# Optimization experiments

Measured on AMD Instinct MI355X. Metric: run time of the kernel, lower is better.

## Reference

```python
import jax, jax.numpy as jnp
import numpy as np

DIM = 512
HEADS = 8
HEAD_DIM = DIM // HEADS
WIN = 3
N = WIN * WIN  # 9 tokens per window
HID = 4 * DIM
B = 8192
SCALE = HEAD_DIM ** -0.5
EPS = 1e-5


def _relative_position_index():
    coords = np.stack(np.meshgrid(np.arange(WIN), np.arange(WIN), indexing='ij'))  # (2,W,W)
    flat = coords.reshape(2, -1)  # (2, N)
    rel = flat[:, :, None] - flat[:, None, :]  # (2, N, N)
    rel = rel.transpose(1, 2, 0).copy()  # (N, N, 2)
    rel[:, :, 0] += WIN - 1
    rel[:, :, 1] += WIN - 1
    rel[:, :, 0] *= 2 * WIN - 1
    return rel.sum(-1)  # (N, N) int

REL_IDX = jnp.asarray(_relative_position_index())


def _layernorm(x, g, b):
    mu = jnp.mean(x, axis=-1, keepdims=True)
    var = jnp.mean(jnp.square(x - mu), axis=-1, keepdims=True)
    return (x - mu) * jax.lax.rsqrt(var + EPS) * g + b


def setup_inputs() -> dict:
    key = jax.random.key(0)
    ks = jax.random.split(key, 16)
    f32 = jnp.float32
    return {
        'x': jax.random.normal(ks[0], (B, N, DIM), f32),
        'gamma1': jnp.ones((DIM,), f32),
        'beta1': jnp.zeros((DIM,), f32),
        'w_qkv': jax.random.normal(ks[1], (3 * DIM, DIM), f32) * 0.02,
        'b_qkv': jnp.zeros((3 * DIM,), f32),
        'bias_table': jax.random.normal(ks[2], ((2 * WIN - 1) ** 2, HEADS), f32) * 0.02,
        'w_proj': jax.random.normal(ks[3], (DIM, DIM), f32) * 0.02,
        'b_proj': jnp.zeros((DIM,), f32),
        'gamma2': jnp.ones((DIM,), f32),
        'beta2': jnp.zeros((DIM,), f32),
        'w_fc1': jax.random.normal(ks[4], (HID, DIM), f32) * 0.02,
        'b_fc1': jnp.zeros((HID,), f32),
        'w_fc2': jax.random.normal(ks[5], (DIM, HID), f32) * 0.02,
        'b_fc2': jnp.zeros((DIM,), f32),
        'w_conv': jax.random.normal(ks[6], (DIM, 1, WIN, WIN), f32) * 0.02,
        'b_conv': jnp.zeros((DIM,), f32),
    }


def reference(x, gamma1, beta1, w_qkv, b_qkv, bias_table, w_proj, b_proj,
              gamma2, beta2, w_fc1, b_fc1, w_fc2, b_fc2, w_conv, b_conv):
    Bn, Nn, C = x.shape
    # --- window attention ---
    shortcut = x
    h = _layernorm(x, gamma1, beta1)
    qkv = h @ w_qkv.T + b_qkv  # (B, N, 3C)
    qkv = qkv.reshape(Bn, Nn, 3, HEADS, HEAD_DIM).transpose(2, 0, 3, 1, 4)  # (3,B,H,N,d)
    q, k, v = qkv[0] * SCALE, qkv[1], qkv[2]
    attn = jnp.einsum('bhnd,bhmd->bhnm', q, k)  # (B,H,N,N)
    rel_bias = bias_table[REL_IDX.reshape(-1)].reshape(Nn, Nn, HEADS).transpose(2, 0, 1)  # (H,N,N)
    attn = jax.nn.softmax(attn + rel_bias[None], axis=-1)
    out = jnp.einsum('bhnm,bhmd->bhnd', attn, v)  # (B,H,N,d)
    out = out.transpose(0, 2, 1, 3).reshape(Bn, Nn, C)
    out = out @ w_proj.T + b_proj
    x = shortcut + out
    # --- MLP ---
    h = _layernorm(x, gamma2, beta2)
    h = jax.nn.gelu(h @ w_fc1.T + b_fc1, approximate=False)
    h = h @ w_fc2.T + b_fc2
    x = x + h
    # --- depthwise 3x3 merge conv over the 3x3 grid (valid -> 1x1) ---
    x4 = x.transpose(0, 2, 1).reshape(Bn, C, WIN, WIN)  # (B,C,3,3)
    y = jnp.einsum('bchw,chw->bc', x4, w_conv[:, 0]) + b_conv  # (B,C)
    return y[:, None, :]  # (B,1,C)
```

## Files before the change

kernel.cpp:

```cpp
#include <hip/hip_runtime.h>


typedef short short8 __attribute__((ext_vector_type(8)));
typedef unsigned short ushort8 __attribute__((ext_vector_type(8)));
typedef float floatx4 __attribute__((ext_vector_type(4)));

static constexpr int R_TOT = 73728;

__device__ __forceinline__ unsigned short f2bf(float f) {
  union { float f; unsigned int u; } v; v.f = f;
  unsigned int r = v.u + 0x7FFFu + ((v.u >> 16) & 1u);
  return (unsigned short)(r >> 16);
}
__device__ __forceinline__ float bf2f(unsigned short u) {
  union { unsigned int u; float f; } v; v.u = ((unsigned int)u) << 16;
  return v.f;
}

__device__ __forceinline__ void gload_lds16(const void* g, void* l) {
  __builtin_amdgcn_global_load_lds(
      (const __attribute__((address_space(1))) unsigned int*)g,
      (__attribute__((address_space(3))) unsigned int*)l, 16, 0, 0);
}

__global__ __launch_bounds__(256)
void cvt4(const float* __restrict__ in, unsigned short* __restrict__ out) {
  int i = (blockIdx.x * 256 + threadIdx.x) * 4;
  floatx4 v = *(const floatx4*)(in + i);
  union { unsigned short s[4]; unsigned long long u; } pk;
  pk.s[0] = f2bf(v[0]); pk.s[1] = f2bf(v[1]); pk.s[2] = f2bf(v[2]); pk.s[3] = f2bf(v[3]);
  *(unsigned long long*)(out + i) = pk.u;
}

__global__ __launch_bounds__(256)
void ln_bf16(const float* __restrict__ in, const float* __restrict__ g,
             const float* __restrict__ b, unsigned short* __restrict__ out) {
  const int lane = threadIdx.x & 63;
  const int wid = threadIdx.x >> 6;
  const size_t row = (size_t)blockIdx.x * 4 + wid;
  const float* p = in + row * 512 + lane * 8;
  floatx4 v0 = *(const floatx4*)p;
  floatx4 v1 = *(const floatx4*)(p + 4);
  float s = v0[0] + v0[1] + v0[2] + v0[3] + v1[0] + v1[1] + v1[2] + v1[3];
  float ss = v0[0]*v0[0] + v0[1]*v0[1] + v0[2]*v0[2] + v0[3]*v0[3]
           + v1[0]*v1[0] + v1[1]*v1[1] + v1[2]*v1[2] + v1[3]*v1[3];
  #pragma unroll
  for (int m = 1; m < 64; m <<= 1) { s += __shfl_xor(s, m); ss += __shfl_xor(ss, m); }
  float mu = s * (1.f / 512.f);
  float var = ss * (1.f / 512.f) - mu * mu;
  float rs = rsqrtf(var + 1e-5f);
  const float* gp = g + lane * 8;
  const float* bp = b + lane * 8;
  floatx4 g0 = *(const floatx4*)gp, g1 = *(const floatx4*)(gp + 4);
  floatx4 b0 = *(const floatx4*)bp, b1 = *(const floatx4*)(bp + 4);
  ushort8 o;
  o[0] = f2bf((v0[0] - mu) * rs * g0[0] + b0[0]);
  o[1] = f2bf((v0[1] - mu) * rs * g0[1] + b0[1]);
  o[2] = f2bf((v0[2] - mu) * rs * g0[2] + b0[2]);
  o[3] = f2bf((v0[3] - mu) * rs * g0[3] + b0[3]);
  o[4] = f2bf((v1[0] - mu) * rs * g1[0] + b1[0]);
  o[5] = f2bf((v1[1] - mu) * rs * g1[1] + b1[1]);
  o[6] = f2bf((v1[2] - mu) * rs * g1[2] + b1[2]);
  o[7] = f2bf((v1[3] - mu) * rs * g1[3] + b1[3]);
  *(ushort8*)(out + row * 512 + lane * 8) = o;
}

template <int EPI>
__global__ __launch_bounds__(256)
void gemm_bt(const unsigned short* __restrict__ A,
             const unsigned short* __restrict__ W,
             const float* __restrict__ bias,
             const float* __restrict__ resid,
             unsigned short* __restrict__ outb,
             float* __restrict__ outf,
             int K, int Nn) {
  __shared__ unsigned short As[128 * 64];
  __shared__ unsigned short Bs[128 * 64];

  const int t = threadIdx.x;
  const int lane = t & 63;
  const int wid = t >> 6;
  const int wr = wid >> 1;
  const int wc = wid & 1;

  const size_t rowB = (size_t)blockIdx.y * 128;
  const size_t colB = (size_t)blockIdx.x * 128;

  floatx4 acc[4][4];
  #pragma unroll
  for (int m = 0; m < 4; ++m)
    #pragma unroll
    for (int n = 0; n < 4; ++n)
      acc[m][n] = (floatx4){0.f, 0.f, 0.f, 0.f};

  const int ar = t >> 3;
  const int ac = (t & 7) * 8;
  const unsigned short* Abase = A + (rowB + ar) * (size_t)K + ac;
  const unsigned short* Wbase = W + (colB + ar) * (size_t)K + ac;
  const size_t K32 = (size_t)K * 32;

  const int la = lane & 15;
  const int lk = (lane >> 4) * 8;

  for (int ks = 0; ks < K; ks += 64) {
    #pragma unroll
    for (int c = 0; c < 4; ++c) {
      gload_lds16(Abase + ks + c * K32, &As[c * 2048 + t * 8]);
      gload_lds16(Wbase + ks + c * K32, &Bs[c * 2048 + t * 8]);
    }
    __syncthreads();
    #pragma unroll
    for (int kk = 0; kk < 2; ++kk) {
      short8 aF[4], bF[4];
      #pragma unroll
      for (int m = 0; m < 4; ++m)
        aF[m] = *(const short8*)&As[(wr * 64 + m * 16 + la) * 64 + kk * 32 + lk];
      #pragma unroll
      for (int n = 0; n < 4; ++n)
        bF[n] = *(const short8*)&Bs[(wc * 64 + n * 16 + la) * 64 + kk * 32 + lk];
      #pragma unroll
      for (int m = 0; m < 4; ++m)
        #pragma unroll
        for (int n = 0; n < 4; ++n)
          acc[m][n] = __builtin_amdgcn_mfma_f32_16x16x32_bf16(aF[m], bF[n], acc[m][n], 0, 0, 0);
    }
    __syncthreads();
  }

  const int r0 = (int)rowB + wr * 64;
  const int c0 = (int)colB + wc * 64;
  #pragma unroll
  for (int m = 0; m < 4; ++m) {
    #pragma unroll
    for (int n = 0; n < 4; ++n) {
      #pragma unroll
      for (int j = 0; j < 4; ++j) {
        int r = r0 + m * 16 + (lane >> 4) * 4 + j;
        int c = c0 + n * 16 + la;
        float v = acc[m][n][j] + bias[c];
        if (EPI == 1) v = 0.5f * v * (1.0f + erff(v * 0.70710678118654752f));
        if (EPI == 2) {
          v += resid[(size_t)r * Nn + c];
          outf[(size_t)r * Nn + c] = v;
        } else {
          outb[(size_t)r * Nn + c] = f2bf(v);
        }
      }
    }
  }
}

__global__ __launch_bounds__(256)
void attn9(const unsigned short* __restrict__ qkv,
           const float* __restrict__ bias_table,
           unsigned short* __restrict__ out) {
  __shared__ float qL[4][9][64];
  __shared__ float kL[4][9][64];
  __shared__ float vL[4][9][64];
  __shared__ float sL[4][9][10];

  const int lane = threadIdx.x & 63;
  const int wid = threadIdx.x >> 6;
  const int bh = blockIdx.x * 4 + wid;
  const int b = bh >> 3;
  const int h = bh & 7;

  const size_t base = (size_t)b * 9 * 1536 + h * 64 + lane;
  #pragma unroll
  for (int i = 0; i < 9; ++i) {
    qL[wid][i][lane] = bf2f(qkv[base + i * 1536]) * 0.125f;
    kL[wid][i][lane] = bf2f(qkv[base + i * 1536 + 512]);
    vL[wid][i][lane] = bf2f(qkv[base + i * 1536 + 1024]);
  }
  __syncthreads();

  #pragma unroll
  for (int p = 0; p < 2; ++p) {
    int pair = lane + p * 64;
    if (pair < 81) {
      int i = pair / 9, j = pair % 9;
      const floatx4* qi = (const floatx4*)qL[wid][i];
      const floatx4* kj = (const floatx4*)kL[wid][j];
      float dot = 0.f;
      #pragma unroll
      for (int d = 0; d < 16; ++d) {
        floatx4 a = qi[d], c = kj[d];
        dot += a[0]*c[0] + a[1]*c[1] + a[2]*c[2] + a[3]*c[3];
      }
      int dy = i / 3 - j / 3 + 2;
      int dx = i % 3 - j % 3 + 2;
      dot += bias_table[(dy * 5 + dx) * 8 + h];
      sL[wid][i][j] = dot;
    }
  }
  __syncthreads();

  if (lane < 9) {
    float m = -1e30f;
    #pragma unroll
    for (int j = 0; j < 9; ++j) m = fmaxf(m, sL[wid][lane][j]);
    float e[9], sum = 0.f;
    #pragma unroll
    for (int j = 0; j < 9; ++j) { e[j] = __expf(sL[wid][lane][j] - m); sum += e[j]; }
    float inv = 1.f / sum;
    #pragma unroll
    for (int j = 0; j < 9; ++j) sL[wid][lane][j] = e[j] * inv;
  }
  __syncthreads();

  const size_t obase = (size_t)b * 9 * 512 + h * 64 + lane;
  #pragma unroll
  for (int i = 0; i < 9; ++i) {
    float a = 0.f;
    #pragma unroll
    for (int j = 0; j < 9; ++j) a += sL[wid][i][j] * vL[wid][j][lane];
    out[obase + i * 512] = f2bf(a);
  }
}

__global__ __launch_bounds__(256)
void dwconv9(const float* __restrict__ x2, const float* __restrict__ wc,
             const float* __restrict__ bc, float* __restrict__ out) {
  int idx = blockIdx.x * 256 + threadIdx.x;
  int c = idx & 511;
  int b = idx >> 9;
  const float* xp = x2 + (size_t)b * 9 * 512 + c;
  float acc = bc[c];
  #pragma unroll
  for (int t = 0; t < 9; ++t) acc += xp[t * 512] * wc[c * 9 + t];
  out[idx] = acc;
}

extern "C" void kernel_launch(void* const* d_in, const int* in_sizes, int n_in,
                              void* d_out, int out_size, void* d_ws, size_t ws_size,
                              hipStream_t stream) {
  const float* x      = (const float*)d_in[0];
  const float* gamma1 = (const float*)d_in[1];
  const float* beta1  = (const float*)d_in[2];
  const float* w_qkv  = (const float*)d_in[3];
  const float* b_qkv  = (const float*)d_in[4];
  const float* bias_t = (const float*)d_in[5];
  const float* w_proj = (const float*)d_in[6];
  const float* b_proj = (const float*)d_in[7];
  const float* gamma2 = (const float*)d_in[8];
  const float* beta2  = (const float*)d_in[9];
  const float* w_fc1  = (const float*)d_in[10];
  const float* b_fc1  = (const float*)d_in[11];
  const float* w_fc2  = (const float*)d_in[12];
  const float* b_fc2  = (const float*)d_in[13];
  const float* w_conv = (const float*)d_in[14];
  const float* b_conv = (const float*)d_in[15];
  float* out = (float*)d_out;

  static const int cand[6] = {73728, 36864, 18432, 9216, 4608, 2304};
  int M_C = 2304;
  for (int i = 0; i < 6; ++i) {
    size_t need = 6291456ull + (size_t)cand[i] * 10240ull;
    if (need <= ws_size) { M_C = cand[i]; break; }
  }
  const int nChunks = R_TOT / M_C;
  const int winC = M_C / 9;

  char* ws = (char*)d_ws;
  unsigned short* wqkvb  = (unsigned short*)(ws);
  unsigned short* wprojb = (unsigned short*)(ws + 1572864);
  unsigned short* wfc1b  = (unsigned short*)(ws + 2097152);
  unsigned short* wfc2b  = (unsigned short*)(ws + 4194304);
  char* base = ws + 6291456;
  const size_t szHB  = (size_t)M_C * 1024;
  const size_t szQKV = (size_t)M_C * 3072;
  const size_t szX1  = (size_t)M_C * 2048;
  unsigned short* hb   = (unsigned short*)base;
  unsigned short* aob  = hb;
  unsigned short* qkvb = (unsigned short*)(base + szHB);
  unsigned short* h2b  = qkvb;
  float* x2            = (float*)(base + szHB + szHB);
  float* x1            = (float*)(base + szHB + szQKV);
  unsigned short* gb   = (unsigned short*)(base + szHB + szQKV + szX1);

  cvt4<<<768, 256, 0, stream>>>(w_qkv, wqkvb);
  cvt4<<<256, 256, 0, stream>>>(w_proj, wprojb);
  cvt4<<<1024, 256, 0, stream>>>(w_fc1, wfc1b);
  cvt4<<<1024, 256, 0, stream>>>(w_fc2, wfc2b);

  for (int ch = 0; ch < nChunks; ++ch) {
    const size_t rOff = (size_t)ch * M_C;
    const float* xC = x + rOff * 512;
    float* outC = out + (size_t)ch * winC * 512;
    const int mt = M_C / 128;

    ln_bf16<<<M_C / 4, 256, 0, stream>>>(xC, gamma1, beta1, hb);
    gemm_bt<0><<<dim3(12, mt), 256, 0, stream>>>(hb, wqkvb, b_qkv, nullptr, qkvb, nullptr, 512, 1536);
    attn9<<<winC * 2, 256, 0, stream>>>(qkvb, bias_t, aob);
    gemm_bt<2><<<dim3(4, mt), 256, 0, stream>>>(aob, wprojb, b_proj, xC, nullptr, x1, 512, 512);
    ln_bf16<<<M_C / 4, 256, 0, stream>>>(x1, gamma2, beta2, h2b);
    gemm_bt<1><<<dim3(16, mt), 256, 0, stream>>>(h2b, wfc1b, b_fc1, nullptr, gb, nullptr, 512, 2048);
    gemm_bt<2><<<dim3(4, mt), 256, 0, stream>>>(gb, wfc2b, b_fc2, x1, nullptr, x2, 2048, 512);
    dwconv9<<<winC * 2, 256, 0, stream>>>(x2, w_conv, b_conv, outC);
  }
}
```

Before: 1.473 ms.

## Replace GEMM with 256x256 double-buffered 8-wave pipelined MFMA kernel

Replaces the simple 128x128 single-buffered GEMM with a 256x256-tile, 512-thread kernel. It double-buffers LDS through direct global-to-LDS loads, swizzles LDS addresses to avoid bank conflicts, interleaves quarter-tile staging with MFMA bursts under s_setprio, and remaps workgroups across XCDs for L2 locality. The goal is to hide global load latency and raise MFMA utilisation in the four GEMMs that dominate runtime. It costs 128KB of LDS per block and much more register pressure, and the hand-placed vmcnt waits and barriers are fragile. It also requires K to be a multiple of 128 and M and N to be multiples of 256.

```diff
diff --git a/kernel.cpp b/kernel.cpp
--- a/kernel.cpp
+++ b/kernel.cpp
@@ -22,6 +22,12 @@
       (const __attribute__((address_space(1))) unsigned int*)g,
       (__attribute__((address_space(3))) unsigned int*)l, 16, 0, 0);
 }
+
+#define FENCE asm volatile("" ::: "memory")
+#define BAR do { FENCE; __builtin_amdgcn_s_barrier(); FENCE; } while (0)
+#define WAITV0 asm volatile("s_waitcnt vmcnt(0)" ::: "memory")
+#define WAITV4 asm volatile("s_waitcnt vmcnt(4)" ::: "memory")
+#define WAITV8 asm volatile("s_waitcnt vmcnt(8)" ::: "memory")
 
 __global__ __launch_bounds__(256)
 void cvt4(const float* __restrict__ in, unsigned short* __restrict__ out) {
@@ -65,85 +71,146 @@
   *(ushort8*)(out + row * 512 + lane * 8) = o;
 }
 
+
+#define STAGE_A(d, qq, tk) do { \
+  gload_lds16(Ap + (rowB + (qq)*64 + rowU) * (size_t)K + (tk) + kofsU, \
+              sm + (d)*32768 + (qq)*16384 + wid*1024); \
+  gload_lds16(Ap + (rowB + 128 + (qq)*64 + rowU) * (size_t)K + (tk) + kofsU, \
+              sm + (d)*32768 + (qq)*16384 + 8192 + wid*1024); \
+} while (0)
+
+#define STAGE_B(d, hb, tk) do { \
+  gload_lds16(Wp + (colB + (wid>>2)*64 + (hb)*32 + colU) * (size_t)K + (tk) + kofsU, \
+              sm + 65536 + (d)*32768 + (hb)*16384 + wid*1024); \
+  gload_lds16(Wp + (colB + (2 + (wid>>2))*64 + (hb)*32 + colU) * (size_t)K + (tk) + kofsU, \
+              sm + 65536 + (d)*32768 + (hb)*16384 + 8192 + wid*1024); \
+} while (0)
+
+#define LOAD_A(d, qq) do { \
+  _Pragma("unroll") \
+  for (int fl = 0; fl < 4; ++fl) { \
+    aF[fl][0] = *(const short8*)(sm + (d)*32768 + (qq)*16384 + wm*8192 + (fl*2+0)*1024 + laneRD); \
+    aF[fl][1] = *(const short8*)(sm + (d)*32768 + (qq)*16384 + wm*8192 + (fl*2+1)*1024 + laneRD); \
+  } \
+} while (0)
+
+#define LOAD_B(d, hb, BF) do { \
+  _Pragma("unroll") \
+  for (int nl = 0; nl < 2; ++nl) { \
+    BF[nl][0] = *(const short8*)(sm + 65536 + (d)*32768 + (hb)*16384 + wn*4096 + (nl*2+0)*1024 + laneRD); \
+    BF[nl][1] = *(const short8*)(sm + 65536 + (d)*32768 + (hb)*16384 + wn*4096 + (nl*2+1)*1024 + laneRD); \
+  } \
+} while (0)
+
+#define MMQ(qa, hb, BF) do { \
+  __builtin_amdgcn_s_setprio(1); \
+  _Pragma("unroll") \
+  for (int fl = 0; fl < 4; ++fl) \
+    _Pragma("unroll") \
+    for (int nl = 0; nl < 2; ++nl) { \
+      acc[(qa)*4+fl][(hb)*2+nl] = __builtin_amdgcn_mfma_f32_16x16x32_bf16(aF[fl][0], BF[nl][0], acc[(qa)*4+fl][(hb)*2+nl], 0, 0, 0); \
+      acc[(qa)*4+fl][(hb)*2+nl] = __builtin_amdgcn_mfma_f32_16x16x32_bf16(aF[fl][1], BF[nl][1], acc[(qa)*4+fl][(hb)*2+nl], 0, 0, 0); \
+    } \
+  __builtin_amdgcn_s_setprio(0); \
+} while (0)
+
 template <int EPI>
-__global__ __launch_bounds__(256)
-void gemm_bt(const unsigned short* __restrict__ A,
-             const unsigned short* __restrict__ W,
-             const float* __restrict__ bias,
-             const float* __restrict__ resid,
-             unsigned short* __restrict__ outb,
-             float* __restrict__ outf,
-             int K, int Nn) {
-  __shared__ unsigned short As[128 * 64];
-  __shared__ unsigned short Bs[128 * 64];
+__global__ __launch_bounds__(512, 2)
+void gemm8p(const unsigned short* __restrict__ Ap,
+            const unsigned short* __restrict__ Wp,
+            const float* __restrict__ bias,
+            const float* __restrict__ resid,
+            unsigned short* __restrict__ outb,
+            float* __restrict__ outf,
+            int K, int Nn, int ntn) {
+  __shared__ __align__(16) char sm[131072];
 
   const int t = threadIdx.x;
-  const int lane = t & 63;
+  const int l = t & 63;
   const int wid = t >> 6;
-  const int wr = wid >> 1;
-  const int wc = wid & 1;
-
-  const size_t rowB = (size_t)blockIdx.y * 128;
-  const size_t colB = (size_t)blockIdx.x * 128;
-
-  floatx4 acc[4][4];
-  #pragma unroll
-  for (int m = 0; m < 4; ++m)
+  const int wm = wid >> 2;
+  const int wn = wid & 3;
+
+  const int nwg = gridDim.x;
+  const int orig = blockIdx.x;
+  const int q8 = nwg >> 3, r8 = nwg & 7;
+  const int xcd = orig & 7, idx = orig >> 3;
+  const int wg = (xcd < r8 ? xcd * (q8 + 1) : r8 * (q8 + 1) + (xcd - r8) * q8) + idx;
+  const int tm = wg / ntn, tn = wg % ntn;
+  const size_t rowB = (size_t)tm * 256;
+  const size_t colB = (size_t)tn * 256;
+
+  const int rowU = (wid >> 1) * 16 + (l >> 2);
+  const int colU = ((wid >> 1) & 1) * 16 + (l >> 2);
+  const int kofsU = (wid & 1) * 32 + (((l & 3) ^ ((l >> 4) & 3)) * 8);
+  const int laneRD = (l & 15) * 64 + (((l >> 4) ^ ((l >> 2) & 3)) * 16);
+
+  floatx4 acc[8][4];
+  #pragma unroll
+  for (int m = 0; m < 8; ++m)
     #pragma unroll
     for (int n = 0; n < 4; ++n)
       acc[m][n] = (floatx4){0.f, 0.f, 0.f, 0.f};
 
-  const int ar = t >> 3;
-  const int ac = (t & 7) * 8;
-  const unsigned short* Abase = A + (rowB + ar) * (size_t)K + ac;
-  const unsigned short* Wbase = W + (colB + ar) * (size_t)K + ac;
-  const size_t K32 = (size_t)K * 32;
-
-  const int la = lane & 15;
-  const int lk = (lane >> 4) * 8;
-
-  for (int ks = 0; ks < K; ks += 64) {
-    #pragma unroll
-    for (int c = 0; c < 4; ++c) {
-      gload_lds16(Abase + ks + c * K32, &As[c * 2048 + t * 8]);
-      gload_lds16(Wbase + ks + c * K32, &Bs[c * 2048 + t * 8]);
-    }
-    __syncthreads();
-    #pragma unroll
-    for (int kk = 0; kk < 2; ++kk) {
-      short8 aF[4], bF[4];
-      #pragma unroll
-      for (int m = 0; m < 4; ++m)
-        aF[m] = *(const short8*)&As[(wr * 64 + m * 16 + la) * 64 + kk * 32 + lk];
-      #pragma unroll
-      for (int n = 0; n < 4; ++n)
-        bF[n] = *(const short8*)&Bs[(wc * 64 + n * 16 + la) * 64 + kk * 32 + lk];
-      #pragma unroll
-      for (int m = 0; m < 4; ++m)
-        #pragma unroll
-        for (int n = 0; n < 4; ++n)
-          acc[m][n] = __builtin_amdgcn_mfma_f32_16x16x32_bf16(aF[m], bF[n], acc[m][n], 0, 0, 0);
-    }
-    __syncthreads();
-  }
-
-  const int r0 = (int)rowB + wr * 64;
-  const int c0 = (int)colB + wc * 64;
-  #pragma unroll
-  for (int m = 0; m < 4; ++m) {
-    #pragma unroll
-    for (int n = 0; n < 4; ++n) {
+  short8 aF[4][2], bF0[2][2], bF1[2][2];
+
+  STAGE_A(0, 0, 0);  STAGE_A(0, 1, 0);  STAGE_B(0, 0, 0);  STAGE_B(0, 1, 0);
+  STAGE_A(1, 0, 64); STAGE_A(1, 1, 64); STAGE_B(1, 0, 64); STAGE_B(1, 1, 64);
+  WAITV8; BAR;
+
+  const int NI = K >> 7;
+  for (int i = 0; i < NI; ++i) {
+    const int tk1 = i * 128 + 64;
+    const int tk2 = i * 128 + 128;
+    const int tk3 = i * 128 + 192;
+    const bool pre = (i > 0);
+    const bool nxt = (i < NI - 1);
+
+    LOAD_A(0, 0); LOAD_B(0, 0, bF0);
+    if (pre) STAGE_A(1, 1, tk1);
+    BAR; MMQ(0, 0, bF0); BAR;
+    LOAD_B(0, 1, bF1);
+    if (pre) STAGE_B(1, 0, tk1);
+    BAR; MMQ(0, 1, bF1); BAR;
+    LOAD_A(0, 1);
+    if (nxt) STAGE_A(0, 0, tk2);
+    BAR; MMQ(1, 1, bF1); BAR;
+    if (nxt) STAGE_B(0, 1, tk2);
+    BAR; MMQ(1, 0, bF0);
+    if (nxt) { WAITV4; } else { WAITV0; }
+    BAR;
+    LOAD_A(1, 0); LOAD_B(1, 0, bF0);
+    if (nxt) STAGE_A(0, 1, tk2);
+    BAR; MMQ(0, 0, bF0); BAR;
+    LOAD_B(1, 1, bF1);
+    if (nxt) STAGE_B(0, 0, tk2);
+    BAR; MMQ(0, 1, bF1); BAR;
+    LOAD_A(1, 1);
+    if (nxt) STAGE_A(1, 0, tk3);
+    BAR; MMQ(1, 1, bF1); BAR;
+    if (nxt) STAGE_B(1, 1, tk3);
+    BAR; MMQ(1, 0, bF0);
+    if (nxt) { WAITV4; }
+    BAR;
+  }
+  FENCE;
+
+  #pragma unroll
+  for (int mi = 0; mi < 8; ++mi) {
+    #pragma unroll
+    for (int ni = 0; ni < 4; ++ni) {
+      const int rr = (int)rowB + wm * 128 + (mi >> 2) * 64 + (mi & 3) * 16 + (l >> 4) * 4;
+      const int cc = (int)colB + wn * 64 + (ni >> 1) * 32 + (ni & 1) * 16 + (l & 15);
+      const float bs = bias[cc];
       #pragma unroll
       for (int j = 0; j < 4; ++j) {
-        int r = r0 + m * 16 + (lane >> 4) * 4 + j;
-        int c = c0 + n * 16 + la;
-        float v = acc[m][n][j] + bias[c];
+        float v = acc[mi][ni][j] + bs;
         if (EPI == 1) v = 0.5f * v * (1.0f + erff(v * 0.70710678118654752f));
         if (EPI == 2) {
-          v += resid[(size_t)r * Nn + c];
-          outf[(size_t)r * Nn + c] = v;
+          v += resid[(size_t)(rr + j) * Nn + cc];
+          outf[(size_t)(rr + j) * Nn + cc] = v;
         } else {
-          outb[(size_t)r * Nn + c] = f2bf(v);
+          outb[(size_t)(rr + j) * Nn + cc] = f2bf(v);
         }
       }
     }
@@ -283,19 +350,19 @@
   cvt4<<<1024, 256, 0, stream>>>(w_fc1, wfc1b);
   cvt4<<<1024, 256, 0, stream>>>(w_fc2, wfc2b);
 
+  const int mt256 = M_C / 256;
   for (int ch = 0; ch < nChunks; ++ch) {
     const size_t rOff = (size_t)ch * M_C;
     const float* xC = x + rOff * 512;
     float* outC = out + (size_t)ch * winC * 512;
-    const int mt = M_C / 128;
 
     ln_bf16<<<M_C / 4, 256, 0, stream>>>(xC, gamma1, beta1, hb);
-    gemm_bt<0><<<dim3(12, mt), 256, 0, stream>>>(hb, wqkvb, b_qkv, nullptr, qkvb, nullptr, 512, 1536);
+    gemm8p<0><<<dim3(mt256 * 6), 512, 0, stream>>>(hb, wqkvb, b_qkv, nullptr, qkvb, nullptr, 512, 1536, 6);
     attn9<<<winC * 2, 256, 0, stream>>>(qkvb, bias_t, aob);
-    gemm_bt<2><<<dim3(4, mt), 256, 0, stream>>>(aob, wprojb, b_proj, xC, nullptr, x1, 512, 512);
+    gemm8p<2><<<dim3(mt256 * 2), 512, 0, stream>>>(aob, wprojb, b_proj, xC, nullptr, x1, 512, 512, 2);
     ln_bf16<<<M_C / 4, 256, 0, stream>>>(x1, gamma2, beta2, h2b);
-    gemm_bt<1><<<dim3(16, mt), 256, 0, stream>>>(h2b, wfc1b, b_fc1, nullptr, gb, nullptr, 512, 2048);
-    gemm_bt<2><<<dim3(4, mt), 256, 0, stream>>>(gb, wfc2b, b_fc2, x1, nullptr, x2, 2048, 512);
+    gemm8p<1><<<dim3(mt256 * 8), 512, 0, stream>>>(h2b, wfc1b, b_fc1, nullptr, gb, nullptr, 512, 2048, 8);
+    gemm8p<2><<<dim3(mt256 * 2), 512, 0, stream>>>(gb, wfc2b, b_fc2, x1, nullptr, x2, 2048, 512, 2);
     dwconv9<<<winC * 2, 256, 0, stream>>>(x2, w_conv, b_conv, outC);
   }
 }
```

Result: faster. 1.372 ms (-6.8%).

## Rewrite bf16 GEMM with 128x256 tiles, swizzled LDS, prefetch and XCD remap

Applied to the files above, without the earlier changes.

Replaces the 128x128, 256-thread GEMM with a 512-thread kernel that computes 128x256 output tiles. It uses an XOR-swizzled LDS layout to avoid bank conflicts and remaps the 1D block index so neighbouring tiles land on the same XCD. It reads the whole K-step of fragments into registers, then issues the next tile's global-to-LDS loads so they overlap the MFMA work, and raises wave priority around the MFMA block. This aims to cut LDS conflicts and exposed load latency, and to improve cache reuse. The cost is more registers, and there is a possible race: LDS is overwritten after the fragment reads without a trailing barrier.

```diff
diff --git a/kernel.cpp b/kernel.cpp
--- a/kernel.cpp
+++ b/kernel.cpp
@@ -22,6 +22,10 @@
       (const __attribute__((address_space(1))) unsigned int*)g,
       (__attribute__((address_space(3))) unsigned int*)l, 16, 0, 0);
 }
+
+#define FENCE asm volatile("" ::: "memory")
+#define BAR do { FENCE; __builtin_amdgcn_s_barrier(); FENCE; } while (0)
+#define WAITV0 asm volatile("s_waitcnt vmcnt(0)" ::: "memory")
 
 __global__ __launch_bounds__(256)
 void cvt4(const float* __restrict__ in, unsigned short* __restrict__ out) {
@@ -61,30 +65,41 @@
   o[4] = f2bf((v1[0] - mu) * rs * g1[0] + b1[0]);
   o[5] = f2bf((v1[1] - mu) * rs * g1[1] + b1[1]);
   o[6] = f2bf((v1[2] - mu) * rs * g1[2] + b1[2]);
-  o[7] = f2bf((v1[3] - mu) * rs * g1[3] + b1[3]);
+  o[7] = f2bf((v1[3] - mu) * rs * g1[3] + b1[7-4]);
   *(ushort8*)(out + row * 512 + lane * 8) = o;
 }
 
 template <int EPI>
-__global__ __launch_bounds__(256)
-void gemm_bt(const unsigned short* __restrict__ A,
-             const unsigned short* __restrict__ W,
-             const float* __restrict__ bias,
-             const float* __restrict__ resid,
-             unsigned short* __restrict__ outb,
-             float* __restrict__ outf,
-             int K, int Nn) {
-  __shared__ unsigned short As[128 * 64];
-  __shared__ unsigned short Bs[128 * 64];
+__global__ __launch_bounds__(512, 4)
+void gemmk(const unsigned short* __restrict__ Ap,
+           const unsigned short* __restrict__ Wp,
+           const float* __restrict__ bias,
+           const float* __restrict__ resid,
+           unsigned short* __restrict__ outb,
+           float* __restrict__ outf,
+           int K, int Nn, int ntn) {
+  __shared__ __align__(16) char sm[49152];
 
   const int t = threadIdx.x;
-  const int lane = t & 63;
+  const int l = t & 63;
   const int wid = t >> 6;
-  const int wr = wid >> 1;
-  const int wc = wid & 1;
-
-  const size_t rowB = (size_t)blockIdx.y * 128;
-  const size_t colB = (size_t)blockIdx.x * 128;
+  const int wm = wid >> 2;
+  const int wn = wid & 3;
+
+  const int nwg = gridDim.x;
+  const int orig = blockIdx.x;
+  const int q8 = nwg >> 3, r8 = nwg & 7;
+  const int xcd = orig & 7, idx = orig >> 3;
+  const int wg = (xcd < r8 ? xcd * (q8 + 1) : r8 * (q8 + 1) + (xcd - r8) * q8) + idx;
+  const int tm = wg / ntn, tn = wg % ntn;
+  const size_t rowB = (size_t)tm * 128;
+  const size_t colB = (size_t)tn * 256;
+
+  const int srow = l >> 3;
+  const int sko = ((l & 7) ^ (l >> 3)) * 8;
+  const int arow = l & 15;
+  const int aoff0 = arow * 128 + (((l >> 4) + 0) ^ (arow & 7)) * 16;
+  const int aoff1 = arow * 128 + (((l >> 4) + 4) ^ (arow & 7)) * 16;
 
   floatx4 acc[4][4];
   #pragma unroll
@@ -93,57 +108,73 @@
     for (int n = 0; n < 4; ++n)
       acc[m][n] = (floatx4){0.f, 0.f, 0.f, 0.f};
 
-  const int ar = t >> 3;
-  const int ac = (t & 7) * 8;
-  const unsigned short* Abase = A + (rowB + ar) * (size_t)K + ac;
-  const unsigned short* Wbase = W + (colB + ar) * (size_t)K + ac;
-  const size_t K32 = (size_t)K * 32;
-
-  const int la = lane & 15;
-  const int lk = (lane >> 4) * 8;
-
-  for (int ks = 0; ks < K; ks += 64) {
-    #pragma unroll
-    for (int c = 0; c < 4; ++c) {
-      gload_lds16(Abase + ks + c * K32, &As[c * 2048 + t * 8]);
-      gload_lds16(Wbase + ks + c * K32, &Bs[c * 2048 + t * 8]);
-    }
-    __syncthreads();
-    #pragma unroll
-    for (int kk = 0; kk < 2; ++kk) {
-      short8 aF[4], bF[4];
-      #pragma unroll
-      for (int m = 0; m < 4; ++m)
-        aF[m] = *(const short8*)&As[(wr * 64 + m * 16 + la) * 64 + kk * 32 + lk];
-      #pragma unroll
-      for (int n = 0; n < 4; ++n)
-        bF[n] = *(const short8*)&Bs[(wc * 64 + n * 16 + la) * 64 + kk * 32 + lk];
-      #pragma unroll
-      for (int m = 0; m < 4; ++m)
-        #pragma unroll
-        for (int n = 0; n < 4; ++n)
-          acc[m][n] = __builtin_amdgcn_mfma_f32_16x16x32_bf16(aF[m], bF[n], acc[m][n], 0, 0, 0);
-    }
-    __syncthreads();
-  }
-
-  const int r0 = (int)rowB + wr * 64;
-  const int c0 = (int)colB + wc * 64;
-  #pragma unroll
-  for (int m = 0; m < 4; ++m) {
-    #pragma unroll
-    for (int n = 0; n < 4; ++n) {
+  const int NI = K >> 6;
+
+  #pragma unroll
+  for (int j = 0; j < 2; ++j)
+    gload_lds16(Ap + (rowB + wid * 16 + j * 8 + srow) * (size_t)K + sko,
+                sm + wid * 2048 + j * 1024);
+  #pragma unroll
+  for (int j = 0; j < 4; ++j)
+    gload_lds16(Wp + (colB + wid * 32 + j * 8 + srow) * (size_t)K + sko,
+                sm + 16384 + wid * 4096 + j * 1024);
+
+  for (int kt = 0; kt < NI; ++kt) {
+    WAITV0;
+    BAR;
+
+    short8 aF[4][2], bF[4][2];
+    #pragma unroll
+    for (int mi = 0; mi < 4; ++mi) {
+      aF[mi][0] = *(const short8*)(sm + wm * 8192 + mi * 2048 + aoff0);
+      aF[mi][1] = *(const short8*)(sm + wm * 8192 + mi * 2048 + aoff1);
+    }
+    #pragma unroll
+    for (int ni = 0; ni < 4; ++ni) {
+      bF[ni][0] = *(const short8*)(sm + 16384 + wn * 8192 + ni * 2048 + aoff0);
+      bF[ni][1] = *(const short8*)(sm + 16384 + wn * 8192 + ni * 2048 + aoff1);
+    }
+
+    if (kt + 1 < NI) {
+      const int tk = (kt + 1) << 6;
+      #pragma unroll
+      for (int j = 0; j < 2; ++j)
+        gload_lds16(Ap + (rowB + wid * 16 + j * 8 + srow) * (size_t)K + tk + sko,
+                    sm + wid * 2048 + j * 1024);
+      #pragma unroll
+      for (int j = 0; j < 4; ++j)
+        gload_lds16(Wp + (colB + wid * 32 + j * 8 + srow) * (size_t)K + tk + sko,
+                    sm + 16384 + wid * 4096 + j * 1024);
+    }
+
+    __builtin_amdgcn_s_setprio(1);
+    #pragma unroll
+    for (int mi = 0; mi < 4; ++mi)
+      #pragma unroll
+      for (int ni = 0; ni < 4; ++ni) {
+        acc[mi][ni] = __builtin_amdgcn_mfma_f32_16x16x32_bf16(aF[mi][0], bF[ni][0], acc[mi][ni], 0, 0, 0);
+        acc[mi][ni] = __builtin_amdgcn_mfma_f32_16x16x32_bf16(aF[mi][1], bF[ni][1], acc[mi][ni], 0, 0, 0);
+      }
+    __builtin_amdgcn_s_setprio(0);
+  }
+  FENCE;
+
+  #pragma unroll
+  for (int mi = 0; mi < 4; ++mi) {
+    #pragma unroll
+    for (int ni = 0; ni < 4; ++ni) {
+      const int rr = (int)rowB + wm * 64 + mi * 16 + (l >> 4) * 4;
+      const int cc = (int)colB + wn * 64 + ni * 16 + (l & 15);
+      const float bs = bias[cc];
       #pragma unroll
       for (int j = 0; j < 4; ++j) {
-        int r = r0 + m * 16 + (lane >> 4) * 4 + j;
-        int c = c0 + n * 16 + la;
-        float v = acc[m][n][j] + bias[c];
+        float v = acc[mi][ni][j] + bs;
         if (EPI == 1) v = 0.5f * v * (1.0f + erff(v * 0.70710678118654752f));
         if (EPI == 2) {
-          v += resid[(size_t)r * Nn + c];
-          outf[(size_t)r * Nn + c] = v;
+          v += resid[(size_t)(rr + j) * Nn + cc];
+          outf[(size_t)(rr + j) * Nn + cc] = v;
         } else {
-          outb[(size_t)r * Nn + c] = f2bf(v);
+          outb[(size_t)(rr + j) * Nn + cc] = f2bf(v);
         }
       }
     }
@@ -283,19 +314,19 @@
   cvt4<<<1024, 256, 0, stream>>>(w_fc1, wfc1b);
   cvt4<<<1024, 256, 0, stream>>>(w_fc2, wfc2b);
 
+  const int mt128 = M_C / 128;
   for (int ch = 0; ch < nChunks; ++ch) {
     const size_t rOff = (size_t)ch * M_C;
     const float* xC = x + rOff * 512;
     float* outC = out + (size_t)ch * winC * 512;
-    const int mt = M_C / 128;
 
     ln_bf16<<<M_C / 4, 256, 0, stream>>>(xC, gamma1, beta1, hb);
-    gemm_bt<0><<<dim3(12, mt), 256, 0, stream>>>(hb, wqkvb, b_qkv, nullptr, qkvb, nullptr, 512, 1536);
+    gemmk<0><<<dim3(mt128 * 6), 512, 0, stream>>>(hb, wqkvb, b_qkv, nullptr, qkvb, nullptr, 512, 1536, 6);
     attn9<<<winC * 2, 256, 0, stream>>>(qkvb, bias_t, aob);
-    gemm_bt<2><<<dim3(4, mt), 256, 0, stream>>>(aob, wprojb, b_proj, xC, nullptr, x1, 512, 512);
+    gemmk<2><<<dim3(mt128 * 2), 512, 0, stream>>>(aob, wprojb, b_proj, xC, nullptr, x1, 512, 512, 2);
     ln_bf16<<<M_C / 4, 256, 0, stream>>>(x1, gamma2, beta2, h2b);
-    gemm_bt<1><<<dim3(16, mt), 256, 0, stream>>>(h2b, wfc1b, b_fc1, nullptr, gb, nullptr, 512, 2048);
-    gemm_bt<2><<<dim3(4, mt), 256, 0, stream>>>(gb, wfc2b, b_fc2, x1, nullptr, x2, 2048, 512);
+    gemmk<1><<<dim3(mt128 * 8), 512, 0, stream>>>(h2b, wfc1b, b_fc1, nullptr, gb, nullptr, 512, 2048, 8);
+    gemmk<2><<<dim3(mt128 * 2), 512, 0, stream>>>(gb, wfc2b, b_fc2, x1, nullptr, x2, 2048, 512, 2);
     dwconv9<<<winC * 2, 256, 0, stream>>>(x2, w_conv, b_conv, outC);
   }
 }
```

After: 2.762 ms. 87.5% more time.
